# Kernel optimization log

Hardware: AMD Instinct MI355X
Metric: run time of the kernel (lower is better)

Reference implementation:

```python
import jax, jax.numpy as jnp
import numpy as np

L, P = 16384, 512
DT_MIN, DT_MAX = 0.001, 0.1
THRESHOLD = 1.0  # spike threshold assumed for cartesian_spike


def setup_inputs() -> dict:
    key = jax.random.key(0)
    k1, k2, k3, k4, k5, k6 = jax.random.split(key, 6)
    u = jax.random.normal(k1, (L, P), dtype=jnp.float32)
    # Stored Lambda param: [..., 0] = log(-Re(Lambda)) with Re(Lambda) < 0, [..., 1] = Im(Lambda)
    lam_real_neg = jax.random.uniform(k2, (P,), minval=0.1, maxval=1.0)  # -Re(Lambda)
    lam_imag = jax.random.normal(k3, (P,)) * 3.0
    Lambda = jnp.stack([jnp.log(lam_real_neg), lam_imag], axis=-1).astype(jnp.float32)
    # init_log_steps: log(dt) uniform in [log(dt_min), log(dt_max)], shape (P, 1)
    log_step = (np.log(DT_MIN) + jax.random.uniform(k4, (P, 1)) * (np.log(DT_MAX) - np.log(DT_MIN))).astype(jnp.float32)
    V_re = jax.random.normal(k5, (P, P), dtype=jnp.float32) / np.sqrt(P)
    V_im = jax.random.normal(k6, (P, P), dtype=jnp.float32) / np.sqrt(P)
    return {"u": u, "Lambda": Lambda, "log_step": log_step, "V_re": V_re, "V_im": V_im}


def _binop(q_i, q_j):
    A_i, b_i = q_i
    A_j, b_j = q_j
    return (A_j * A_i, A_j * b_i + b_j)


def reference(u, Lambda, log_step, V_re, V_im):
    # keep_imag = False: u stays real. discretization = 'zoh', activation = 'cartesian_spike'.
    Lambda_tilde = -jnp.exp(Lambda[..., 0]) + 1j * Lambda[..., 1]            # (P,) complex
    step = jnp.exp(log_step[:, 0])                                            # (P,)
    Lambda_bar = jnp.exp(Lambda_tilde * step)                                 # (P,) |.|<1
    # B_tilde = I, so zoh gives B_bar = diag((Lambda_bar - 1)/Lambda); B_bar @ u_t = coef * u_t
    B_coef = (Lambda_bar - 1.0) / Lambda_tilde                                # (P,)
    Lambda_elements = jnp.broadcast_to(Lambda_bar, (u.shape[0], Lambda_bar.shape[0]))
    Bu_elements = B_coef[None, :] * u.astype(Lambda_bar.dtype)                # (L, P) complex
    _, xs = jax.lax.associative_scan(_binop, (Lambda_elements, Bu_elements))  # (L, P)
    V = V_re + 1j * V_im
    xs = xs @ V.T                                                             # vmap(V @ x) over L
    spikes = (xs.real > THRESHOLD).astype(jnp.float32)                        # cartesian_spike
    return spikes
```

## Files before the change

kernel.cpp:

```cpp
#include <hip/hip_runtime.h>

#define L_LEN   16384
#define P_DIM   512
#define CHUNK   64
#define NCHUNK  256

#define KDIM    1024
#define NDIM    512
#define BM      128
#define BN      128
#define BK      64

typedef __bf16 bf16_t;
typedef __bf16 bf16x8 __attribute__((ext_vector_type(8)));
typedef float  floatx4 __attribute__((ext_vector_type(4)));

__device__ __forceinline__ void channel_consts(const float* __restrict__ Lam,
                                               const float* __restrict__ lstep,
                                               int p, float& ar, float& ai,
                                               float& br, float& bi) {
    float lr = -expf(Lam[2 * p + 0]);
    float li = Lam[2 * p + 1];
    float s  = expf(lstep[p]);
    float er = expf(lr * s);
    ar = er * cosf(li * s);
    ai = er * sinf(li * s);
    float dr = ar - 1.0f, di = ai;
    float inv = 1.0f / (lr * lr + li * li);
    br = (dr * lr + di * li) * inv;
    bi = (di * lr - dr * li) * inv;
}

__global__ void __launch_bounds__(P_DIM) k_scan_ends(const float* __restrict__ u,
        const float* __restrict__ Lam, const float* __restrict__ lstep,
        float2* __restrict__ endv) {
    int p = threadIdx.x;
    int c = blockIdx.x;
    float ar, ai, br, bi;
    channel_consts(Lam, lstep, p, ar, ai, br, bi);
    float xr = 0.f, xi = 0.f;
    const float* up = u + (size_t)c * CHUNK * P_DIM + p;
    #pragma unroll 8
    for (int k = 0; k < CHUNK; ++k) {
        float uv = up[(size_t)k * P_DIM];
        float nr = ar * xr - ai * xi + br * uv;
        float ni = ar * xi + ai * xr + bi * uv;
        xr = nr; xi = ni;
    }
    endv[c * P_DIM + p] = make_float2(xr, xi);
}

__global__ void __launch_bounds__(P_DIM) k_carry(const float* __restrict__ Lam,
        const float* __restrict__ lstep, const float2* __restrict__ endv,
        float2* __restrict__ carry) {
    int p = threadIdx.x;
    float lr = -expf(Lam[2 * p + 0]);
    float li = Lam[2 * p + 1];
    float s  = expf(lstep[p]);
    float t  = s * (float)CHUNK;
    float er = expf(lr * t);
    float Ar = er * cosf(li * t);
    float Ai = er * sinf(li * t);
    float xr = 0.f, xi = 0.f;
    #pragma unroll 8
    for (int c = 0; c < NCHUNK; ++c) {
        carry[c * P_DIM + p] = make_float2(xr, xi);
        float2 e = endv[c * P_DIM + p];
        float nr = Ar * xr - Ai * xi + e.x;
        float ni = Ar * xi + Ai * xr + e.y;
        xr = nr; xi = ni;
    }
}

__global__ void __launch_bounds__(256) k_bt(const float* __restrict__ Vre,
        const float* __restrict__ Vim, bf16_t* __restrict__ Bt) {
    int idx = blockIdx.x * 256 + threadIdx.x;
    int j = idx >> 9;
    int c = idx & 511;
    union { unsigned int w; bf16_t h[2]; } pk;
    pk.h[0] = (bf16_t)Vre[j * P_DIM + c];
    pk.h[1] = (bf16_t)(-Vim[j * P_DIM + c]);
    ((unsigned int*)Bt)[idx] = pk.w;
}

__global__ void __launch_bounds__(P_DIM) k_materialize(const float* __restrict__ u,
        const float* __restrict__ Lam, const float* __restrict__ lstep,
        const float2* __restrict__ carry, bf16_t* __restrict__ A) {
    int p = threadIdx.x;
    int c = blockIdx.x;
    float ar, ai, br, bi;
    channel_consts(Lam, lstep, p, ar, ai, br, bi);
    float2 x0 = carry[c * P_DIM + p];
    float xr = x0.x, xi = x0.y;
    const float* up = u + (size_t)c * CHUNK * P_DIM + p;
    unsigned int* Ap32 = (unsigned int*)(A + (size_t)c * CHUNK * KDIM);
    #pragma unroll 8
    for (int t = 0; t < CHUNK; ++t) {
        float uv = up[(size_t)t * P_DIM];
        float nr = ar * xr - ai * xi + br * uv;
        float ni = ar * xi + ai * xr + bi * uv;
        xr = nr; xi = ni;
        union { unsigned int w; bf16_t h[2]; } pk;
        pk.h[0] = (bf16_t)xr;
        pk.h[1] = (bf16_t)xi;
        Ap32[(size_t)t * (KDIM / 2) + p] = pk.w;
    }
}

__global__ void __launch_bounds__(256) k_gemm(const bf16_t* __restrict__ A,
        const bf16_t* __restrict__ Bt, float* __restrict__ out) {
    __shared__ __align__(16) bf16_t As[BM * BK];
    __shared__ __align__(16) bf16_t Bs[BN * BK];

    const int tid  = threadIdx.x;
    const int lane = tid & 63;
    const int w    = tid >> 6;
    const int m0   = blockIdx.x * BM;
    const int n0   = blockIdx.y * BN;
    const int wm   = (w >> 1) * 64;
    const int wn   = (w & 1) * 64;
    const int fr_m = lane & 15;
    const int fr_g = lane >> 4;

    floatx4 acc[4][4];
    #pragma unroll
    for (int i = 0; i < 4; ++i)
        #pragma unroll
        for (int j = 0; j < 4; ++j) {
            floatx4 z = {0.f, 0.f, 0.f, 0.f};
            acc[i][j] = z;
        }

    const bf16_t* Asrc = A  + (size_t)m0 * KDIM;
    const bf16_t* Bsrc = Bt + (size_t)n0 * KDIM;

    for (int kt = 0; kt < KDIM; kt += BK) {
        __syncthreads();
        #pragma unroll
        for (int i = 0; i < 4; ++i) {
            const int cb = i * 256 + w * 64;
            const int c  = cb + lane;
            const int r  = c >> 3;
            const int gc = (c & 7) ^ (r & 7);
            const bf16_t* ga = Asrc + (size_t)r * KDIM + kt + gc * 8;
            const bf16_t* gb = Bsrc + (size_t)r * KDIM + kt + gc * 8;
            __builtin_amdgcn_global_load_lds(
                (const __attribute__((address_space(1))) unsigned int*)ga,
                (__attribute__((address_space(3))) unsigned int*)((char*)As + cb * 16),
                16, 0, 0);
            __builtin_amdgcn_global_load_lds(
                (const __attribute__((address_space(1))) unsigned int*)gb,
                (__attribute__((address_space(3))) unsigned int*)((char*)Bs + cb * 16),
                16, 0, 0);
        }
        __syncthreads();

        #pragma unroll
        for (int kk = 0; kk < BK; kk += 32) {
            const int kc = (kk >> 3) + fr_g;
            bf16x8 af[4], bfv[4];
            #pragma unroll
            for (int i = 0; i < 4; ++i) {
                int m = wm + i * 16 + fr_m;
                af[i] = *(const bf16x8*)((const char*)As + m * (BK * 2)
                                         + ((kc ^ (m & 7)) << 4));
            }
            #pragma unroll
            for (int j = 0; j < 4; ++j) {
                int n = wn + j * 16 + fr_m;
                bfv[j] = *(const bf16x8*)((const char*)Bs + n * (BK * 2)
                                          + ((kc ^ (n & 7)) << 4));
            }
            #pragma unroll
            for (int i = 0; i < 4; ++i)
                #pragma unroll
                for (int j = 0; j < 4; ++j)
                    acc[i][j] = __builtin_amdgcn_mfma_f32_16x16x32_bf16(
                        af[i], bfv[j], acc[i][j], 0, 0, 0);
        }
    }

    #pragma unroll
    for (int i = 0; i < 4; ++i)
        #pragma unroll
        for (int j = 0; j < 4; ++j)
            #pragma unroll
            for (int r = 0; r < 4; ++r) {
                int rr = wm + i * 16 + fr_g * 4 + r;
                int cl = wn + j * 16 + fr_m;
                out[(size_t)(m0 + rr) * NDIM + (n0 + cl)] =
                    (acc[i][j][r] > 1.0f) ? 1.0f : 0.0f;
            }
}

extern "C" void kernel_launch(void* const* d_in, const int* in_sizes, int n_in,
                              void* d_out, int out_size, void* d_ws, size_t ws_size,
                              hipStream_t stream) {
    (void)in_sizes; (void)n_in; (void)out_size; (void)ws_size;
    const float* u     = (const float*)d_in[0];
    const float* Lam   = (const float*)d_in[1];
    const float* lstep = (const float*)d_in[2];
    const float* Vre   = (const float*)d_in[3];
    const float* Vim   = (const float*)d_in[4];
    float* out = (float*)d_out;

    char* ws = (char*)d_ws;
    float2* endv  = (float2*)(ws);
    float2* carry = (float2*)(ws + (1 << 20));
    bf16_t* Bt    = (bf16_t*)(ws + (2 << 20));
    bf16_t* A     = (bf16_t*)(ws + (4 << 20));

    hipLaunchKernelGGL(k_scan_ends, dim3(NCHUNK), dim3(P_DIM), 0, stream,
                       u, Lam, lstep, endv);
    hipLaunchKernelGGL(k_bt, dim3(NDIM * P_DIM / 256), dim3(256), 0, stream,
                       Vre, Vim, Bt);
    hipLaunchKernelGGL(k_carry, dim3(1), dim3(P_DIM), 0, stream,
                       Lam, lstep, endv, carry);
    hipLaunchKernelGGL(k_materialize, dim3(NCHUNK), dim3(P_DIM), 0, stream,
                       u, Lam, lstep, carry, A);
    hipLaunchKernelGGL(k_gemm, dim3(L_LEN / BM, NDIM / BN), dim3(256), 0, stream,
                       A, Bt, out);
}
```

Before: 155.6 us.

## Fuse chunked scan, carry and materialize into one single-pass kernel

Replaces the three-kernel chunked scan (chunk ends, serial carry, materialize) plus the separate V-transpose kernel with one kernel. Each chunk block publishes its end state with a flag, waits for all earlier chunks, then combines their aggregates using powers of the chunk transition. The u values are kept in registers so u is read only once. The V conversion runs in extra blocks of the same launch. This removes launch overhead, the single-block serial carry kernel and the second read of u. In exchange it depends on blocks being scheduled forward for the spin-wait, does O(c) work per later chunk, and needs 64 floats of registers per thread.

```diff
diff --git a/kernel.cpp b/kernel.cpp
--- a/kernel.cpp
+++ b/kernel.cpp
@@ -4,6 +4,7 @@
 #define P_DIM   512
 #define CHUNK   64
 #define NCHUNK  256
+#define NBT     8
 
 #define KDIM    1024
 #define NDIM    512
@@ -15,95 +16,103 @@
 typedef __bf16 bf16x8 __attribute__((ext_vector_type(8)));
 typedef float  floatx4 __attribute__((ext_vector_type(4)));
 
-__device__ __forceinline__ void channel_consts(const float* __restrict__ Lam,
-                                               const float* __restrict__ lstep,
-                                               int p, float& ar, float& ai,
-                                               float& br, float& bi) {
+__global__ void __launch_bounds__(512) k_scan_fused(
+        const float* __restrict__ u, const float* __restrict__ Lam,
+        const float* __restrict__ lstep, const float* __restrict__ Vre,
+        const float* __restrict__ Vim, unsigned int* __restrict__ flags,
+        unsigned long long* __restrict__ agg, bf16_t* __restrict__ Bt,
+        bf16_t* __restrict__ A) {
+    const int b   = blockIdx.x;
+    const int tid = threadIdx.x;
+
+    if (b < NBT) {
+        const int base = b * (NDIM * P_DIM / NBT);
+        #pragma unroll 4
+        for (int i = 0; i < NDIM * P_DIM / NBT / 512; ++i) {
+            int idx = base + i * 512 + tid;
+            int j = idx >> 9;
+            int c = idx & 511;
+            union { unsigned int w; bf16_t h[2]; } pk;
+            pk.h[0] = (bf16_t)Vre[j * P_DIM + c];
+            pk.h[1] = (bf16_t)(-Vim[j * P_DIM + c]);
+            ((unsigned int*)Bt)[idx] = pk.w;
+        }
+        return;
+    }
+
+    const int c = b - NBT;
+    const int p = tid;
+
     float lr = -expf(Lam[2 * p + 0]);
     float li = Lam[2 * p + 1];
     float s  = expf(lstep[p]);
     float er = expf(lr * s);
-    ar = er * cosf(li * s);
-    ai = er * sinf(li * s);
+    float ar = er * cosf(li * s);
+    float ai = er * sinf(li * s);
     float dr = ar - 1.0f, di = ai;
     float inv = 1.0f / (lr * lr + li * li);
-    br = (dr * lr + di * li) * inv;
-    bi = (di * lr - dr * li) * inv;
-}
-
-__global__ void __launch_bounds__(P_DIM) k_scan_ends(const float* __restrict__ u,
-        const float* __restrict__ Lam, const float* __restrict__ lstep,
-        float2* __restrict__ endv) {
-    int p = threadIdx.x;
-    int c = blockIdx.x;
-    float ar, ai, br, bi;
-    channel_consts(Lam, lstep, p, ar, ai, br, bi);
+    float br = (dr * lr + di * li) * inv;
+    float bi = (di * lr - dr * li) * inv;
+    float tt = s * (float)CHUNK;
+    float eR = expf(lr * tt);
+    float Ar = eR * cosf(li * tt);
+    float Ai = eR * sinf(li * tt);
+
+    float uv[CHUNK];
+    const float* up = u + (size_t)c * CHUNK * P_DIM + p;
     float xr = 0.f, xi = 0.f;
-    const float* up = u + (size_t)c * CHUNK * P_DIM + p;
-    #pragma unroll 8
-    for (int k = 0; k < CHUNK; ++k) {
-        float uv = up[(size_t)k * P_DIM];
-        float nr = ar * xr - ai * xi + br * uv;
-        float ni = ar * xi + ai * xr + bi * uv;
+    #pragma unroll
+    for (int t = 0; t < CHUNK; ++t) {
+        uv[t] = up[(size_t)t * P_DIM];
+        float nr = ar * xr - ai * xi + br * uv[t];
+        float ni = ar * xi + ai * xr + bi * uv[t];
         xr = nr; xi = ni;
     }
-    endv[c * P_DIM + p] = make_float2(xr, xi);
-}
-
-__global__ void __launch_bounds__(P_DIM) k_carry(const float* __restrict__ Lam,
-        const float* __restrict__ lstep, const float2* __restrict__ endv,
-        float2* __restrict__ carry) {
-    int p = threadIdx.x;
-    float lr = -expf(Lam[2 * p + 0]);
-    float li = Lam[2 * p + 1];
-    float s  = expf(lstep[p]);
-    float t  = s * (float)CHUNK;
-    float er = expf(lr * t);
-    float Ar = er * cosf(li * t);
-    float Ai = er * sinf(li * t);
-    float xr = 0.f, xi = 0.f;
-    #pragma unroll 8
-    for (int c = 0; c < NCHUNK; ++c) {
-        carry[c * P_DIM + p] = make_float2(xr, xi);
-        float2 e = endv[c * P_DIM + p];
-        float nr = Ar * xr - Ai * xi + e.x;
-        float ni = Ar * xi + Ai * xr + e.y;
+
+    union { unsigned long long ull; float f[2]; } pk;
+    pk.f[0] = xr; pk.f[1] = xi;
+    __hip_atomic_store(&agg[(size_t)c * P_DIM + p], pk.ull,
+                       __ATOMIC_RELAXED, __HIP_MEMORY_SCOPE_AGENT);
+    __threadfence();
+    __syncthreads();
+    if (tid == 0)
+        __hip_atomic_store(&flags[c], 1u, __ATOMIC_RELEASE,
+                           __HIP_MEMORY_SCOPE_AGENT);
+
+    float cr = 0.f, ci = 0.f;
+    if (c > 0) {
+        int ok;
+        do {
+            int f = 1;
+            if (tid < c)
+                f = (__hip_atomic_load(&flags[tid], __ATOMIC_ACQUIRE,
+                                       __HIP_MEMORY_SCOPE_AGENT) != 0);
+            ok = __syncthreads_and(f);
+        } while (!ok);
+        float fr = 1.f, fi = 0.f;
+        for (int j = c - 1; j >= 0; --j) {
+            union { unsigned long long ull; float f[2]; } gv;
+            gv.ull = __hip_atomic_load(&agg[(size_t)j * P_DIM + p],
+                                       __ATOMIC_RELAXED, __HIP_MEMORY_SCOPE_AGENT);
+            cr += fr * gv.f[0] - fi * gv.f[1];
+            ci += fr * gv.f[1] + fi * gv.f[0];
+            float nfr = fr * Ar - fi * Ai;
+            float nfi = fr * Ai + fi * Ar;
+            fr = nfr; fi = nfi;
+        }
+    }
+
+    xr = cr; xi = ci;
+    unsigned int* Ap32 = (unsigned int*)(A + (size_t)c * CHUNK * KDIM);
+    #pragma unroll
+    for (int t = 0; t < CHUNK; ++t) {
+        float nr = ar * xr - ai * xi + br * uv[t];
+        float ni = ar * xi + ai * xr + bi * uv[t];
         xr = nr; xi = ni;
-    }
-}
-
-__global__ void __launch_bounds__(256) k_bt(const float* __restrict__ Vre,
-        const float* __restrict__ Vim, bf16_t* __restrict__ Bt) {
-    int idx = blockIdx.x * 256 + threadIdx.x;
-    int j = idx >> 9;
-    int c = idx & 511;
-    union { unsigned int w; bf16_t h[2]; } pk;
-    pk.h[0] = (bf16_t)Vre[j * P_DIM + c];
-    pk.h[1] = (bf16_t)(-Vim[j * P_DIM + c]);
-    ((unsigned int*)Bt)[idx] = pk.w;
-}
-
-__global__ void __launch_bounds__(P_DIM) k_materialize(const float* __restrict__ u,
-        const float* __restrict__ Lam, const float* __restrict__ lstep,
-        const float2* __restrict__ carry, bf16_t* __restrict__ A) {
-    int p = threadIdx.x;
-    int c = blockIdx.x;
-    float ar, ai, br, bi;
-    channel_consts(Lam, lstep, p, ar, ai, br, bi);
-    float2 x0 = carry[c * P_DIM + p];
-    float xr = x0.x, xi = x0.y;
-    const float* up = u + (size_t)c * CHUNK * P_DIM + p;
-    unsigned int* Ap32 = (unsigned int*)(A + (size_t)c * CHUNK * KDIM);
-    #pragma unroll 8
-    for (int t = 0; t < CHUNK; ++t) {
-        float uv = up[(size_t)t * P_DIM];
-        float nr = ar * xr - ai * xi + br * uv;
-        float ni = ar * xi + ai * xr + bi * uv;
-        xr = nr; xi = ni;
-        union { unsigned int w; bf16_t h[2]; } pk;
-        pk.h[0] = (bf16_t)xr;
-        pk.h[1] = (bf16_t)xi;
-        Ap32[(size_t)t * (KDIM / 2) + p] = pk.w;
+        union { unsigned int w; bf16_t h[2]; } o;
+        o.h[0] = (bf16_t)xr;
+        o.h[1] = (bf16_t)xi;
+        Ap32[(size_t)t * (KDIM / 2) + p] = o.w;
     }
 }
 
@@ -205,19 +214,14 @@
     float* out = (float*)d_out;
 
     char* ws = (char*)d_ws;
-    float2* endv  = (float2*)(ws);
-    float2* carry = (float2*)(ws + (1 << 20));
-    bf16_t* Bt    = (bf16_t*)(ws + (2 << 20));
-    bf16_t* A     = (bf16_t*)(ws + (4 << 20));
-
-    hipLaunchKernelGGL(k_scan_ends, dim3(NCHUNK), dim3(P_DIM), 0, stream,
-                       u, Lam, lstep, endv);
-    hipLaunchKernelGGL(k_bt, dim3(NDIM * P_DIM / 256), dim3(256), 0, stream,
-                       Vre, Vim, Bt);
-    hipLaunchKernelGGL(k_carry, dim3(1), dim3(P_DIM), 0, stream,
-                       Lam, lstep, endv, carry);
-    hipLaunchKernelGGL(k_materialize, dim3(NCHUNK), dim3(P_DIM), 0, stream,
-                       u, Lam, lstep, carry, A);
+    unsigned int*       flags = (unsigned int*)(ws);
+    unsigned long long* agg   = (unsigned long long*)(ws + 0x100000);
+    bf16_t*             Bt    = (bf16_t*)(ws + 0x200000);
+    bf16_t*             A     = (bf16_t*)(ws + 0x400000);
+
+    hipMemsetAsync(flags, 0, NCHUNK * sizeof(unsigned int), stream);
+    hipLaunchKernelGGL(k_scan_fused, dim3(NBT + NCHUNK), dim3(512), 0, stream,
+                       u, Lam, lstep, Vre, Vim, flags, agg, Bt, A);
     hipLaunchKernelGGL(k_gemm, dim3(L_LEN / BM, NDIM / BN), dim3(256), 0, stream,
                        A, Bt, out);
 }
```

Result: slower. 210.6 us (+35.4%).
